# Optimization experiments

Measured on AMD Instinct MI355X. Metric: run time of the kernel, lower is better.

Reference implementation:

```python
import jax, jax.numpy as jnp
import numpy as np

EPS = 1e-6  # torch F.pairwise_distance eps, added to the difference elementwise

B, Z = 8192, 128
N_CLASSES = 62
P = int(N_CLASSES * 1.5)  # 93 proxies


def pdist(a, b):
    """||a_i - b_j + EPS||_2 for all pairs, without a [N,M,Z] intermediate.
    Expansion: ||a-b||^2 + 2*EPS*sum(a-b) + Z*EPS^2."""
    aa = jnp.sum(a * a, axis=-1)[:, None]
    bb = jnp.sum(b * b, axis=-1)[None, :]
    ab = a @ b.T
    eps_term = 2.0 * EPS * (jnp.sum(a, -1)[:, None] - jnp.sum(b, -1)[None, :]) + a.shape[-1] * EPS * EPS
    return jnp.sqrt(jnp.maximum(aa + bb - 2.0 * ab + eps_term, 0.0))


def setup_inputs() -> dict:
    key = jax.random.key(0)
    k0, k1, k2 = jax.random.split(key, 3)
    z = jax.random.normal(k0, (B, Z), dtype=jnp.float32)
    y_idx = jax.random.randint(k1, (B,), 0, N_CLASSES, dtype=jnp.int32)
    proxies = jax.random.uniform(k2, (P, Z), dtype=jnp.float32)  # nn.init.uniform_
    y_map = jnp.arange(N_CLASSES, dtype=jnp.int32)  # y_to_relative_y_train (unique classes)
    return {"z": z, "y_idx": y_idx, "proxies": proxies, "y_map": y_map}


def reference(z, y_idx, proxies, y_map):
    # F.normalize(proxies, p=2, dim=-1) with 1e-12 clamp
    prx = proxies / jnp.maximum(jnp.linalg.norm(proxies, axis=-1, keepdims=True), 1e-12)
    # y_rel[j] = position where y_to_relative_y_train == y_idx[j] (exactly one match)
    y_rel = jnp.argmax(y_map[None, :] == y_idx[:, None], axis=-1)  # [B]

    anchors = np.arange(0, z.shape[0] - 3, 3)  # static anchor indices i
    z_a = z[anchors]                            # [A,Z]

    # nearest proxy to each anchor
    D_prox = pdist(z_a, prx)                    # [A,P]
    prox_p = prx[jnp.argmin(D_prox, axis=-1)]   # [A,Z]

    # distance from chosen proxy to every sample; restrict to suffix j>=i with same class
    D_pz = pdist(prox_p, z)                     # [A,B]
    mask = (np.arange(z.shape[0])[None, :] >= anchors[:, None]) & \
           (y_rel[None, :] == y_rel[anchors][:, None])  # [A,B], row i always has j=i True
    D_pos = jnp.where(mask, D_pz, -jnp.inf)
    j_p = jnp.argmax(D_pos, axis=-1)            # hardest positive index
    D_p = jnp.take_along_axis(D_pos, j_p[:, None], axis=-1)[:, 0]  # [A]

    # distances from hardest positive to all proxies -> NCA denominator
    D_n = pdist(z[j_p], prx)                    # [A,P]
    losses = D_p + jax.nn.logsumexp(-D_n, axis=-1)  # -log(exp(-D_p)/sum exp(-D_n))
    return jnp.mean(losses)
```

## Files before the change

### kernel.cpp

```cpp
#include <hip/hip_runtime.h>
#include <math.h>

#define B_N   8192
#define Z_D   128
#define P_N   93
#define NCLS  62
#define A_N   2730
#define BCAP  256
#define GT_S  96
#define NPART 683
#define TWO_EPS   2e-6f
#define ZEPS2     (128.0f * 1e-6f * 1e-6f)


#define AT_LD(p)      __hip_atomic_load((p), __ATOMIC_RELAXED, __HIP_MEMORY_SCOPE_AGENT)
#define AT_ST(p, v)   __hip_atomic_store((p), (v), __ATOMIC_RELAXED, __HIP_MEMORY_SCOPE_AGENT)
#define AT_ADDU(p, v) __hip_atomic_fetch_add((p), (v), __ATOMIC_RELAXED, __HIP_MEMORY_SCOPE_AGENT)

__device__ __forceinline__ float wave_sum(float v) {
#pragma unroll
  for (int off = 1; off < 64; off <<= 1) v += __shfl_xor(v, off, 64);
  return v;
}
__device__ __forceinline__ float wave_min(float v) {
#pragma unroll
  for (int off = 1; off < 64; off <<= 1) v = fminf(v, __shfl_xor(v, off, 64));
  return v;
}

__global__ __launch_bounds__(512) void kA(
    const float* __restrict__ z, const int* __restrict__ y_idx,
    const float* __restrict__ prox, const int* __restrict__ y_map,
    float* __restrict__ pp, float* __restrict__ sp,
    float* __restrict__ zz, float* __restrict__ sz, float* __restrict__ w,
    int* __restrict__ cnt, int* __restrict__ bkt, float* __restrict__ GT,
    unsigned int* __restrict__ ctr) {
  __shared__ float linv[6];
  __shared__ float pt[6 * Z_D];
  __shared__ int lcnt;
  const int b = blockIdx.x, tid = threadIdx.x;
  const int lane = tid & 63, wv = tid >> 6;

  if (b == 0 && tid < 17) ctr[tid * 32] = 0u;

  if (b < 256) {
    const int jch = b & 15, kt = b >> 4, k0 = kt * 6;
    const int nk = (kt == 15) ? 3 : 6;
    const int j = jch * 512 + tid;
    const float* __restrict__ zrow = z + (size_t)j * Z_D;
    if (wv < nk) {
      const int k = k0 + wv;
      const float a = prox[k * Z_D + lane];
      const float c = prox[k * Z_D + 64 + lane];
      const float s = wave_sum(a + c);
      const float q = wave_sum(a * a + c * c);
      const float inv = 1.0f / fmaxf(sqrtf(q), 1e-12f);
      if (lane == 0) {
        linv[wv] = inv;
        if (jch == 0) { pp[k] = q * inv * inv; sp[k] = s * inv; }
      }
    }
    __syncthreads();
    {
      const int nf = nk * 32;
      const float4* __restrict__ src = (const float4*)(prox + (size_t)k0 * Z_D);
      for (int t = tid; t < nf; t += 512) {
        const float iv = linv[t >> 5];
        const float4 v = src[t];
        ((float4*)pt)[t] = make_float4(v.x * iv, v.y * iv, v.z * iv, v.w * iv);
      }
    }
    __syncthreads();
    if (kt < 15) {
      float a0 = 0, a1 = 0, a2 = 0, a3 = 0, a4 = 0, a5 = 0;
#pragma unroll 8
      for (int i4 = 0; i4 < Z_D; i4 += 4) {
        const float4 zv = *(const float4*)(zrow + i4);
        const int f = i4 >> 2;
        const float4 q0 = ((const float4*)pt)[0 * 32 + f];
        const float4 q1 = ((const float4*)pt)[1 * 32 + f];
        const float4 q2 = ((const float4*)pt)[2 * 32 + f];
        const float4 q3 = ((const float4*)pt)[3 * 32 + f];
        const float4 q4 = ((const float4*)pt)[4 * 32 + f];
        const float4 q5 = ((const float4*)pt)[5 * 32 + f];
        a0 += zv.x * q0.x + zv.y * q0.y + zv.z * q0.z + zv.w * q0.w;
        a1 += zv.x * q1.x + zv.y * q1.y + zv.z * q1.z + zv.w * q1.w;
        a2 += zv.x * q2.x + zv.y * q2.y + zv.z * q2.z + zv.w * q2.w;
        a3 += zv.x * q3.x + zv.y * q3.y + zv.z * q3.z + zv.w * q3.w;
        a4 += zv.x * q4.x + zv.y * q4.y + zv.z * q4.z + zv.w * q4.w;
        a5 += zv.x * q5.x + zv.y * q5.y + zv.z * q5.z + zv.w * q5.w;
      }
      float* g = GT + (size_t)j * GT_S + k0;
      *(float2*)(g + 0) = make_float2(a0, a1);
      *(float2*)(g + 2) = make_float2(a2, a3);
      *(float2*)(g + 4) = make_float2(a4, a5);
    } else {
      float a0 = 0, a1 = 0, a2 = 0, zs = 0, zq = 0;
#pragma unroll 8
      for (int i4 = 0; i4 < Z_D; i4 += 4) {
        const float4 zv = *(const float4*)(zrow + i4);
        const int f = i4 >> 2;
        const float4 q0 = ((const float4*)pt)[0 * 32 + f];
        const float4 q1 = ((const float4*)pt)[1 * 32 + f];
        const float4 q2 = ((const float4*)pt)[2 * 32 + f];
        zs += zv.x + zv.y + zv.z + zv.w;
        zq += zv.x * zv.x + zv.y * zv.y + zv.z * zv.z + zv.w * zv.w;
        a0 += zv.x * q0.x + zv.y * q0.y + zv.z * q0.z + zv.w * q0.w;
        a1 += zv.x * q1.x + zv.y * q1.y + zv.z * q1.z + zv.w * q1.w;
        a2 += zv.x * q2.x + zv.y * q2.y + zv.z * q2.z + zv.w * q2.w;
      }
      float* g = GT + (size_t)j * GT_S + 90;
      *(float2*)(g) = make_float2(a0, a1);
      g[2] = a2;
      zz[j] = zq;
      sz[j] = zs;
      w[j] = zq - TWO_EPS * zs;
    }
  } else {
    const int c = b - 256;
    if (tid == 0) lcnt = 0;
    __syncthreads();
    const int ym = y_map[c];
    for (int j = tid; j < B_N; j += 512) {
      if (y_idx[j] == ym) {
        const int pos = atomicAdd(&lcnt, 1);
        if (pos < BCAP) bkt[c * BCAP + pos] = j;
      }
    }
    __syncthreads();
    if (tid == 0) cnt[c] = min(lcnt, BCAP);
  }
}

__global__ __launch_bounds__(256) void kB2(
    const int* __restrict__ y_idx, const int* __restrict__ y_map,
    const float* __restrict__ pp, const float* __restrict__ sp,
    const float* __restrict__ zz, const float* __restrict__ sz,
    const float* __restrict__ w,
    const int* __restrict__ cnt, const int* __restrict__ bkt,
    const float* __restrict__ GT, float* partial, unsigned int* ctr,
    float* __restrict__ out) {
  __shared__ float lpp[P_N], lsp[P_N];
  __shared__ int lymap[NCLS];
  __shared__ float part[4];
  const int b = blockIdx.x;
  const int tid = threadIdx.x, lane = tid & 63, wv = tid >> 6;
  if (tid < P_N) { lpp[tid] = pp[tid]; lsp[tid] = sp[tid]; }
  if (tid < NCLS) lymap[tid] = y_map[tid];
  __syncthreads();

  const int wid = b * 4 + wv;
  float loss = 0.0f;
  if (wid < A_N) {
    const int i = 3 * wid;
    const int yi = y_idx[i];
    const unsigned long long mm = __ballot(lane < NCLS && lymap[lane] == yi);
    const int cls = __ffsll(mm) - 1;
    const float zzi = zz[i], szi = sz[i];
    const int kB = lane + 64;

    const int n = cnt[cls];
    const int* __restrict__ bk = bkt + cls * BCAP;
    int pjj[4];
    float pww[4];
#pragma unroll
    for (int r = 0; r < 4; ++r) {
      const int t = lane + (r << 6);
      pjj[r] = (t < n) ? bk[t] : -1;
    }
#pragma unroll
    for (int r = 0; r < 4; ++r)
      pww[r] = (pjj[r] >= i) ? w[pjj[r]] : 0.0f;

    const float* __restrict__ GTi = GT + (size_t)i * GT_S;
    float v1 = fmaxf(zzi + lpp[lane] - 2.0f * GTi[lane] +
                     TWO_EPS * (szi - lsp[lane]) + ZEPS2, 0.0f);
    int i1 = lane;
    if (kB < P_N) {
      const float v2 = fmaxf(zzi + lpp[kB] - 2.0f * GTi[kB] +
                             TWO_EPS * (szi - lsp[kB]) + ZEPS2, 0.0f);
      if (v2 < v1) { v1 = v2; i1 = kB; }
    }
#pragma unroll
    for (int off = 1; off < 64; off <<= 1) {
      const float ov = __shfl_xor(v1, off, 64);
      const int oi = __shfl_xor(i1, off, 64);
      if (ov < v1 || (ov == v1 && oi < i1)) { v1 = ov; i1 = oi; }
    }
    const int p = i1;

    const float cp = lpp[p] + TWO_EPS * lsp[p] + ZEPS2;
    float best = -INFINITY;
    int bestj = 0x7fffffff;
#pragma unroll
    for (int r = 0; r < 4; ++r) {
      const int jj = pjj[r];
      if (jj >= i) {
        const float vv = fmaxf(cp + pww[r] - 2.0f * GT[(size_t)jj * GT_S + p], 0.0f);
        if (vv > best || (vv == best && jj < bestj)) { best = vv; bestj = jj; }
      }
    }
#pragma unroll
    for (int off = 1; off < 64; off <<= 1) {
      const float ov = __shfl_xor(best, off, 64);
      const int oj = __shfl_xor(bestj, off, 64);
      if (ov > best || (ov == best && oj < bestj)) { best = ov; bestj = oj; }
    }
    const float Dp = sqrtf(best);
    const int jp = bestj;

    const float zzj = zz[jp], szj = sz[jp];
    const float* __restrict__ GTj = GT + (size_t)jp * GT_S;
    const float d1 = sqrtf(fmaxf(zzj + lpp[lane] - 2.0f * GTj[lane] +
                                 TWO_EPS * (szj - lsp[lane]) + ZEPS2, 0.0f));
    float d2 = INFINITY;
    if (kB < P_N)
      d2 = sqrtf(fmaxf(zzj + lpp[kB] - 2.0f * GTj[kB] +
                       TWO_EPS * (szj - lsp[kB]) + ZEPS2, 0.0f));
    const float mn = wave_min(fminf(d1, d2));
    float ss = expf(mn - d1) + ((kB < P_N) ? expf(mn - d2) : 0.0f);
    ss = wave_sum(ss);
    loss = Dp - mn + logf(ss);
  }
  if (lane == 0) part[wv] = (wid < A_N) ? loss : 0.0f;
  __syncthreads();

  if (wv == 0) {
    int last = 0;
    if (lane == 0) {
      AT_ST(&partial[b], part[0] + part[1] + part[2] + part[3]);
      __builtin_amdgcn_s_waitcnt(0);
      const int sub = b & 15;
      const unsigned quota = (sub < 11) ? 43u : 42u;
      const unsigned old = AT_ADDU(&ctr[sub * 32], 1u);
      if (old == quota - 1u) {
        const unsigned so = AT_ADDU(&ctr[16 * 32], 1u);
        if (so == 15u) last = 1;
      }
    }
    last = __shfl(last, 0, 64);
    if (last) {
      float s = 0.0f;
#pragma unroll
      for (int r = 0; r < 11; ++r) {
        const int t = lane + r * 64;
        if (t < NPART) s += AT_LD(&partial[t]);
      }
      s = wave_sum(s);
      if (lane == 0) out[0] = s * (1.0f / (float)A_N);
    }
  }
}

extern "C" void kernel_launch(void* const* d_in, const int* in_sizes, int n_in,
                              void* d_out, int out_size, void* d_ws, size_t ws_size,
                              hipStream_t stream) {
  const float* z = (const float*)d_in[0];
  const int* y_idx = (const int*)d_in[1];
  const float* prox = (const float*)d_in[2];
  const int* y_map = (const int*)d_in[3];
  float* out = (float*)d_out;

  char* ws = (char*)d_ws;
  unsigned int* ctr = (unsigned int*)(ws + 0);
  float* pp    = (float*)(ws + 2560);
  float* sp    = (float*)(ws + 3072);
  float* zz    = (float*)(ws + 3584);
  float* sz    = (float*)(ws + 36352);
  float* w     = (float*)(ws + 69120);
  int*   cnt   = (int*)  (ws + 101888);
  int*   bkt   = (int*)  (ws + 102144);
  float* parts = (float*)(ws + 165632);
  float* GT    = (float*)(ws + 168448);

  kA<<<256 + NCLS, 512, 0, stream>>>(z, y_idx, prox, y_map,
                                     pp, sp, zz, sz, w, cnt, bkt, GT, ctr);
  kB2<<<NPART, 256, 0, stream>>>(y_idx, y_map, pp, sp, zz, sz, w,
                                 cnt, bkt, GT, parts, ctr, out);
}
```

Baseline: 81.53 us.

## Transpose z into workspace and precompute normalized proxies before GEMV kernel

Adds a pre-pass kernel that transposes z into a column-major buffer and writes normalized proxies plus their norm and sum terms. The z·proxy kernel then reads z with coalesced per-thread loads and skips the per-block proxy normalization in LDS. This removes strided row loads and repeated normalization work. The cost is an extra launch and roughly 4 MB of extra global writes and reads for zT. The new path runs only when the workspace is large enough and falls back to the old kernel otherwise.

```diff
diff --git a/kernel.cpp b/kernel.cpp
--- a/kernel.cpp
+++ b/kernel.cpp
@@ -28,7 +28,130 @@
   return v;
 }
 
-__global__ __launch_bounds__(512) void kA(
+__global__ __launch_bounds__(256) void kT(
+    const float* __restrict__ z, const float* __restrict__ prox,
+    float* __restrict__ zT, float* __restrict__ ps,
+    float* __restrict__ pp, float* __restrict__ sp) {
+  __shared__ float4 lds[32][33];
+  const int b = blockIdx.x, tid = threadIdx.x;
+  const int j0 = b * 32;
+#pragma unroll
+  for (int k = 0; k < 4; ++k) {
+    const int g = tid + k * 256;
+    const int r = g >> 5, c = g & 31;
+    lds[r][c] = *(const float4*)(z + (size_t)(j0 + r) * Z_D + c * 4);
+  }
+  __syncthreads();
+  const float* ldsF = (const float*)lds;
+#pragma unroll
+  for (int k2 = 0; k2 < 4; ++k2) {
+    const int idx = tid + k2 * 256;
+    const int d = idx >> 3, a = idx & 7;
+    float4 v;
+    v.x = ldsF[(4 * a + 0) * 132 + d];
+    v.y = ldsF[(4 * a + 1) * 132 + d];
+    v.z = ldsF[(4 * a + 2) * 132 + d];
+    v.w = ldsF[(4 * a + 3) * 132 + d];
+    *(float4*)(zT + (size_t)d * B_N + j0 + 4 * a) = v;
+  }
+  if (b < P_N && tid < 64) {
+    const int lane = tid;
+    const float a = prox[b * Z_D + lane];
+    const float c2 = prox[b * Z_D + 64 + lane];
+    const float s = wave_sum(a + c2);
+    const float q = wave_sum(a * a + c2 * c2);
+    const float inv = 1.0f / fmaxf(sqrtf(q), 1e-12f);
+    if (lane == 0) { pp[b] = q * inv * inv; sp[b] = s * inv; }
+    if (lane < 32) {
+      const float4 v = *(const float4*)(prox + b * Z_D + lane * 4);
+      *(float4*)(ps + b * Z_D + lane * 4) =
+          make_float4(v.x * inv, v.y * inv, v.z * inv, v.w * inv);
+    }
+  }
+}
+
+__global__ __launch_bounds__(512) void kA_t(
+    const float* __restrict__ zT, const int* __restrict__ y_idx,
+    const float* __restrict__ ps, const int* __restrict__ y_map,
+    float* __restrict__ zz, float* __restrict__ sz, float* __restrict__ w,
+    int* __restrict__ cnt, int* __restrict__ bkt, float* __restrict__ GT,
+    unsigned int* __restrict__ ctr) {
+  __shared__ int lcnt;
+  const int b = blockIdx.x, tid = threadIdx.x;
+
+  if (b == 0 && tid < 17) ctr[tid * 32] = 0u;
+
+  if (b < 256) {
+    const int jch = b & 15, kt = b >> 4, k0 = kt * 6;
+    const int j = jch * 512 + tid;
+    const float* __restrict__ zc = zT + j;
+    const float* __restrict__ p0 = ps + (size_t)k0 * Z_D;
+    if (kt < 15) {
+      float a0 = 0, a1 = 0, a2 = 0, a3 = 0, a4 = 0, a5 = 0;
+#pragma unroll 8
+      for (int g = 0; g < 32; ++g) {
+        const float zv0 = zc[(size_t)(4 * g + 0) * B_N];
+        const float zv1 = zc[(size_t)(4 * g + 1) * B_N];
+        const float zv2 = zc[(size_t)(4 * g + 2) * B_N];
+        const float zv3 = zc[(size_t)(4 * g + 3) * B_N];
+        const float4 q0 = *(const float4*)(p0 + 0 * Z_D + 4 * g);
+        const float4 q1 = *(const float4*)(p0 + 1 * Z_D + 4 * g);
+        const float4 q2 = *(const float4*)(p0 + 2 * Z_D + 4 * g);
+        const float4 q3 = *(const float4*)(p0 + 3 * Z_D + 4 * g);
+        const float4 q4 = *(const float4*)(p0 + 4 * Z_D + 4 * g);
+        const float4 q5 = *(const float4*)(p0 + 5 * Z_D + 4 * g);
+        a0 += zv0 * q0.x + zv1 * q0.y + zv2 * q0.z + zv3 * q0.w;
+        a1 += zv0 * q1.x + zv1 * q1.y + zv2 * q1.z + zv3 * q1.w;
+        a2 += zv0 * q2.x + zv1 * q2.y + zv2 * q2.z + zv3 * q2.w;
+        a3 += zv0 * q3.x + zv1 * q3.y + zv2 * q3.z + zv3 * q3.w;
+        a4 += zv0 * q4.x + zv1 * q4.y + zv2 * q4.z + zv3 * q4.w;
+        a5 += zv0 * q5.x + zv1 * q5.y + zv2 * q5.z + zv3 * q5.w;
+      }
+      float* g = GT + (size_t)j * GT_S + k0;
+      *(float2*)(g + 0) = make_float2(a0, a1);
+      *(float2*)(g + 2) = make_float2(a2, a3);
+      *(float2*)(g + 4) = make_float2(a4, a5);
+    } else {
+      float a0 = 0, a1 = 0, a2 = 0, zs = 0, zq = 0;
+#pragma unroll 8
+      for (int g = 0; g < 32; ++g) {
+        const float zv0 = zc[(size_t)(4 * g + 0) * B_N];
+        const float zv1 = zc[(size_t)(4 * g + 1) * B_N];
+        const float zv2 = zc[(size_t)(4 * g + 2) * B_N];
+        const float zv3 = zc[(size_t)(4 * g + 3) * B_N];
+        const float4 q0 = *(const float4*)(p0 + 0 * Z_D + 4 * g);
+        const float4 q1 = *(const float4*)(p0 + 1 * Z_D + 4 * g);
+        const float4 q2 = *(const float4*)(p0 + 2 * Z_D + 4 * g);
+        zs += zv0 + zv1 + zv2 + zv3;
+        zq += zv0 * zv0 + zv1 * zv1 + zv2 * zv2 + zv3 * zv3;
+        a0 += zv0 * q0.x + zv1 * q0.y + zv2 * q0.z + zv3 * q0.w;
+        a1 += zv0 * q1.x + zv1 * q1.y + zv2 * q1.z + zv3 * q1.w;
+        a2 += zv0 * q2.x + zv1 * q2.y + zv2 * q2.z + zv3 * q2.w;
+      }
+      float* g = GT + (size_t)j * GT_S + 90;
+      *(float2*)(g) = make_float2(a0, a1);
+      g[2] = a2;
+      zz[j] = zq;
+      sz[j] = zs;
+      w[j] = zq - TWO_EPS * zs;
+    }
+  } else {
+    const int c = b - 256;
+    if (tid == 0) lcnt = 0;
+    __syncthreads();
+    const int ym = y_map[c];
+    for (int j = tid; j < B_N; j += 512) {
+      if (y_idx[j] == ym) {
+        const int pos = atomicAdd(&lcnt, 1);
+        if (pos < BCAP) bkt[c * BCAP + pos] = j;
+      }
+    }
+    __syncthreads();
+    if (tid == 0) cnt[c] = min(lcnt, BCAP);
+  }
+}
+
+__global__ __launch_bounds__(512) void kA_l(
     const float* __restrict__ z, const int* __restrict__ y_idx,
     const float* __restrict__ prox, const int* __restrict__ y_map,
     float* __restrict__ pp, float* __restrict__ sp,
@@ -272,9 +395,17 @@
   int*   bkt   = (int*)  (ws + 102144);
   float* parts = (float*)(ws + 165632);
   float* GT    = (float*)(ws + 168448);
-
-  kA<<<256 + NCLS, 512, 0, stream>>>(z, y_idx, prox, y_map,
-                                     pp, sp, zz, sz, w, cnt, bkt, GT, ctr);
+  float* zT    = (float*)(ws + 3314176);
+  float* psc   = (float*)(ws + 7508480);
+
+  if (ws_size >= (size_t)7556096) {
+    kT<<<256, 256, 0, stream>>>(z, prox, zT, psc, pp, sp);
+    kA_t<<<256 + NCLS, 512, 0, stream>>>(zT, y_idx, psc, y_map,
+                                         zz, sz, w, cnt, bkt, GT, ctr);
+  } else {
+    kA_l<<<256 + NCLS, 512, 0, stream>>>(z, y_idx, prox, y_map, pp, sp,
+                                         zz, sz, w, cnt, bkt, GT, ctr);
+  }
   kB2<<<NPART, 256, 0, stream>>>(y_idx, y_map, pp, sp, zz, sz, w,
                                  cnt, bkt, GT, parts, ctr, out);
 }
```

New measurement: 88.69 us. 8.8% more time.
